# Optimization experiments

Hardware: AMD Instinct MI355X
Metric: run time of the kernel (lower is better)

## Reference

```python
import jax, jax.numpy as jnp
import numpy as np
import math

DM, DP, P = 1024, 128, 256
B, S = 8, 4096

def setup_inputs() -> dict:
    key = jax.random.key(0)
    ks = jax.random.split(key, 7)
    sd = lambda fan_in: 1.0 / math.sqrt(fan_in)
    return {
        "x": jax.random.normal(ks[0], (B, S, DM), jnp.float32),
        "prim_embeds": jax.random.normal(ks[1], (P, DP), jnp.float32),
        "Wq": jax.random.normal(ks[2], (DP, DM), jnp.float32) * sd(DM),
        "Wk": jax.random.normal(ks[3], (DP, DP), jnp.float32) * sd(DP),
        "Wv": jax.random.normal(ks[4], (DP, DP), jnp.float32) * sd(DP),
        "Wo": jax.random.normal(ks[5], (DM, DP), jnp.float32) * sd(DP),
        "gate_w": jax.random.normal(ks[6], (1, DM), jnp.float32) * sd(DM),
        "gate_b": jnp.zeros((1,), jnp.float32),
    }

def reference(x, prim_embeds, Wq, Wk, Wv, Wo, gate_w, gate_b):
    # q: [B,S,dp]; k,v: [P,dp]
    q = jnp.einsum('bsm,pm->bsp', x, Wq)          # p here = d_prim
    k = prim_embeds @ Wk.T                         # [P, dp]
    v = prim_embeds @ Wv.T                         # [P, dp]
    scale = 1.0 / math.sqrt(q.shape[-1])
    scores = jnp.einsum('bsd,pd->bsp', q, k) * scale  # [B,S,P]
    attn = jax.nn.softmax(scores, axis=-1)
    ctx = jnp.einsum('bsp,pd->bsd', attn, v)       # [B,S,dp]
    out = jnp.einsum('bsd,md->bsm', ctx, Wo)       # [B,S,dm]
    gate = jax.nn.sigmoid(jnp.einsum('bsm,om->bso', x, gate_w) + gate_b)  # [B,S,1]
    return gate * out
```

## Files before the change

### kernel.cpp

```cpp
#include <hip/hip_runtime.h>
#include <hip/hip_bf16.h>

typedef unsigned short ushort_t;
typedef __attribute__((ext_vector_type(8))) short short8;
typedef __attribute__((ext_vector_type(8))) unsigned short ushort8;
typedef __attribute__((ext_vector_type(4))) float f32x4;

#define MFMA16(a, b, c) __builtin_amdgcn_mfma_f32_16x16x32_bf16((a), (b), (c), 0, 0, 0)

__device__ __forceinline__ ushort_t f2bf(float f) {
  unsigned int u = __builtin_bit_cast(unsigned int, f);
  u += 0x7FFFu + ((u >> 16) & 1u);
  return (ushort_t)(u >> 16);
}

#define DMdim 1024
#define DPdim 128
#define PPdim 256

#define WQ_ROWS 144
#define WQ_EXT_OFF 0
#define WO_OFF (WQ_ROWS * DMdim)
#define KB_OFF (WO_OFF + DMdim * DPdim)
#define VT_OFF (KB_OFF + PPdim * DPdim)

__global__ void prep_kernel(const float* __restrict__ Wq, const float* __restrict__ Wk,
                            const float* __restrict__ Wv, const float* __restrict__ Wo,
                            const float* __restrict__ gate_w, const float* __restrict__ prim,
                            ushort_t* __restrict__ ws) {
  int idx = blockIdx.x * 256 + threadIdx.x;
  if (idx < WQ_ROWS * DMdim) {
    int r = idx >> 10, m = idx & (DMdim - 1);
    float v = (r < DPdim) ? Wq[r * DMdim + m] : (r == DPdim ? gate_w[m] : 0.f);
    ws[WQ_EXT_OFF + idx] = f2bf(v);
    return;
  }
  idx -= WQ_ROWS * DMdim;
  if (idx < DMdim * DPdim) { ws[WO_OFF + idx] = f2bf(Wo[idx]); return; }
  idx -= DMdim * DPdim;
  if (idx < PPdim * DPdim) {
    int p = idx >> 7, d = idx & (DPdim - 1);
    float s = 0.f;
    for (int j = 0; j < DPdim; ++j) s += prim[p * DPdim + j] * Wk[d * DPdim + j];
    ws[KB_OFF + idx] = f2bf(s);
    return;
  }
  idx -= PPdim * DPdim;
  if (idx < PPdim * DPdim) {
    int p = idx >> 7, d = idx & (DPdim - 1);
    float s = 0.f;
    for (int j = 0; j < DPdim; ++j) s += prim[p * DPdim + j] * Wv[d * DPdim + j];
    ws[VT_OFF + d * PPdim + p] = f2bf(s);
  }
}

#define LDX 72
#define LDQ 136
#define LDA 264
#define LDC 136

__global__ __launch_bounds__(256, 2) void fused_kernel(
    const float* __restrict__ x, const float* __restrict__ gate_b,
    const ushort_t* __restrict__ ws, float* __restrict__ out)
{
  __shared__ __align__(16) ushort_t smem[64 * LDA];
  __shared__ float gate_lds[64];

  const ushort_t* wq_ext = ws + WQ_EXT_OFF;
  const ushort_t* wo_b   = ws + WO_OFF;
  const ushort_t* k_b    = ws + KB_OFF;
  const ushort_t* v_t    = ws + VT_OFF;

  const int tid  = threadIdx.x;
  const int wid  = tid >> 6;
  const int lane = tid & 63;
  const int quad = lane >> 4;
  const int l16  = lane & 15;
  const int tok0 = blockIdx.x * 64;

  f32x4 qacc[9];
  #pragma unroll
  for (int ct = 0; ct < 9; ++ct) qacc[ct] = (f32x4){0.f, 0.f, 0.f, 0.f};

  const int srow = tid >> 2, sseg = tid & 3;

  for (int kc = 0; kc < DMdim; kc += 64) {
    const float4* xv = reinterpret_cast<const float4*>(
        x + (tok0 + srow) * DMdim + kc + sseg * 16);
    float4 f0 = xv[0], f1 = xv[1], f2 = xv[2], f3 = xv[3];
    ushort8 u0, u1;
    u0[0]=f2bf(f0.x); u0[1]=f2bf(f0.y); u0[2]=f2bf(f0.z); u0[3]=f2bf(f0.w);
    u0[4]=f2bf(f1.x); u0[5]=f2bf(f1.y); u0[6]=f2bf(f1.z); u0[7]=f2bf(f1.w);
    u1[0]=f2bf(f2.x); u1[1]=f2bf(f2.y); u1[2]=f2bf(f2.z); u1[3]=f2bf(f2.w);
    u1[4]=f2bf(f3.x); u1[5]=f2bf(f3.y); u1[6]=f2bf(f3.z); u1[7]=f2bf(f3.w);
    *reinterpret_cast<ushort8*>(&smem[srow * LDX + sseg * 16])     = u0;
    *reinterpret_cast<ushort8*>(&smem[srow * LDX + sseg * 16 + 8]) = u1;
    __syncthreads();
    #pragma unroll
    for (int ks = 0; ks < 2; ++ks) {
      short8 a = *reinterpret_cast<const short8*>(
          &smem[(wid * 16 + l16) * LDX + ks * 32 + quad * 8]);
      #pragma unroll
      for (int ct = 0; ct < 9; ++ct) {
        short8 b = *reinterpret_cast<const short8*>(
            &wq_ext[(ct * 16 + l16) * DMdim + kc + ks * 32 + quad * 8]);
        qacc[ct] = MFMA16(a, b, qacc[ct]);
      }
    }
    __syncthreads();
  }

  #pragma unroll
  for (int ct = 0; ct < 8; ++ct)
    #pragma unroll
    for (int r = 0; r < 4; ++r)
      smem[(wid * 16 + quad * 4 + r) * LDQ + ct * 16 + l16] = f2bf(qacc[ct][r]);
  if (l16 == 0) {
    float gb = gate_b[0];
    #pragma unroll
    for (int r = 0; r < 4; ++r) {
      float lg = qacc[8][r] + gb;
      gate_lds[wid * 16 + quad * 4 + r] = 1.f / (1.f + __expf(-lg));
    }
  }
  __syncthreads();

  short8 qa[4];
  #pragma unroll
  for (int k4 = 0; k4 < 4; ++k4)
    qa[k4] = *reinterpret_cast<const short8*>(
        &smem[(wid * 16 + l16) * LDQ + k4 * 32 + quad * 8]);

  f32x4 sacc[16];
  #pragma unroll
  for (int ct = 0; ct < 16; ++ct) sacc[ct] = (f32x4){0.f, 0.f, 0.f, 0.f};
  #pragma unroll
  for (int ct = 0; ct < 16; ++ct)
    #pragma unroll
    for (int k4 = 0; k4 < 4; ++k4) {
      short8 b = *reinterpret_cast<const short8*>(
          &k_b[(ct * 16 + l16) * DPdim + k4 * 32 + quad * 8]);
      sacc[ct] = MFMA16(qa[k4], b, sacc[ct]);
    }

  const float SC = 0.08838834764831845f * 1.44269504088896f;
  float rmax[4], rsum[4], inv[4];
  #pragma unroll
  for (int r = 0; r < 4; ++r) rmax[r] = -3.0e38f;
  #pragma unroll
  for (int ct = 0; ct < 16; ++ct)
    #pragma unroll
    for (int r = 0; r < 4; ++r) rmax[r] = fmaxf(rmax[r], sacc[ct][r]);
  #pragma unroll
  for (int m = 1; m < 16; m <<= 1)
    #pragma unroll
    for (int r = 0; r < 4; ++r) rmax[r] = fmaxf(rmax[r], __shfl_xor(rmax[r], m, 64));
  #pragma unroll
  for (int r = 0; r < 4; ++r) rsum[r] = 0.f;
  #pragma unroll
  for (int ct = 0; ct < 16; ++ct)
    #pragma unroll
    for (int r = 0; r < 4; ++r) {
      float e = exp2f((sacc[ct][r] - rmax[r]) * SC);
      sacc[ct][r] = e;
      rsum[r] += e;
    }
  #pragma unroll
  for (int m = 1; m < 16; m <<= 1)
    #pragma unroll
    for (int r = 0; r < 4; ++r) rsum[r] += __shfl_xor(rsum[r], m, 64);
  #pragma unroll
  for (int r = 0; r < 4; ++r) inv[r] = 1.f / rsum[r];

  __syncthreads();
  #pragma unroll
  for (int ct = 0; ct < 16; ++ct)
    #pragma unroll
    for (int r = 0; r < 4; ++r)
      smem[(wid * 16 + quad * 4 + r) * LDA + ct * 16 + l16] = f2bf(sacc[ct][r]);
  __syncthreads();

  short8 pa[8];
  #pragma unroll
  for (int k8 = 0; k8 < 8; ++k8)
    pa[k8] = *reinterpret_cast<const short8*>(
        &smem[(wid * 16 + l16) * LDA + k8 * 32 + quad * 8]);
  f32x4 cacc[8];
  #pragma unroll
  for (int ct = 0; ct < 8; ++ct) cacc[ct] = (f32x4){0.f, 0.f, 0.f, 0.f};
  #pragma unroll
  for (int ct = 0; ct < 8; ++ct)
    #pragma unroll
    for (int k8 = 0; k8 < 8; ++k8) {
      short8 b = *reinterpret_cast<const short8*>(
          &v_t[(ct * 16 + l16) * PPdim + k8 * 32 + quad * 8]);
      cacc[ct] = MFMA16(pa[k8], b, cacc[ct]);
    }
  __syncthreads();
  #pragma unroll
  for (int ct = 0; ct < 8; ++ct)
    #pragma unroll
    for (int r = 0; r < 4; ++r)
      smem[(wid * 16 + quad * 4 + r) * LDC + ct * 16 + l16] =
          f2bf(cacc[ct][r] * inv[r]);
  __syncthreads();

  short8 ca[4];
  #pragma unroll
  for (int k4 = 0; k4 < 4; ++k4)
    ca[k4] = *reinterpret_cast<const short8*>(
        &smem[(wid * 16 + l16) * LDC + k4 * 32 + quad * 8]);
  float g[4];
  #pragma unroll
  for (int r = 0; r < 4; ++r) g[r] = gate_lds[wid * 16 + quad * 4 + r];

  for (int mc = 0; mc < DMdim; mc += 128) {
    f32x4 oacc[8];
    #pragma unroll
    for (int ct = 0; ct < 8; ++ct) oacc[ct] = (f32x4){0.f, 0.f, 0.f, 0.f};
    #pragma unroll
    for (int ct = 0; ct < 8; ++ct)
      #pragma unroll
      for (int k4 = 0; k4 < 4; ++k4) {
        short8 b = *reinterpret_cast<const short8*>(
            &wo_b[(mc + ct * 16 + l16) * DPdim + k4 * 32 + quad * 8]);
        oacc[ct] = MFMA16(ca[k4], b, oacc[ct]);
      }
    #pragma unroll
    for (int ct = 0; ct < 8; ++ct)
      #pragma unroll
      for (int r = 0; r < 4; ++r)
        out[(tok0 + wid * 16 + quad * 4 + r) * DMdim + mc + ct * 16 + l16] =
            oacc[ct][r] * g[r];
  }
}

extern "C" void kernel_launch(void* const* d_in, const int* in_sizes, int n_in,
                              void* d_out, int out_size, void* d_ws, size_t ws_size,
                              hipStream_t stream) {
  const float* x    = (const float*)d_in[0];
  const float* prim = (const float*)d_in[1];
  const float* Wq   = (const float*)d_in[2];
  const float* Wk   = (const float*)d_in[3];
  const float* Wv   = (const float*)d_in[4];
  const float* Wo   = (const float*)d_in[5];
  const float* gw   = (const float*)d_in[6];
  const float* gb   = (const float*)d_in[7];
  float* out = (float*)d_out;
  ushort_t* ws = (ushort_t*)d_ws;

  prep_kernel<<<344064 / 256, 256, 0, stream>>>(Wq, Wk, Wv, Wo, gw, prim, ws);
  fused_kernel<<<512, 256, 0, stream>>>(x, gb, ws, out);
}
```

Before: 377.8 us.

## Split fused kernel into attention and output-projection kernels with per-wave LDS slabs

Splits the single fused kernel into an attention kernel, which writes bf16 context and gate values to workspace, and a separate output-projection kernel that uses more blocks and higher occupancy. In the attention kernel each wave now loads x directly into MFMA operand registers, which removes the LDS staging and the block-wide barriers. It also gives each wave its own LDS slab. The prep kernel's K/V projections are vectorized with float4. In exchange, the context and gate take an extra round trip through global memory, and per-wave x loads are less coalesced.

```diff
diff --git a/kernel.cpp b/kernel.cpp
--- a/kernel.cpp
+++ b/kernel.cpp
@@ -3,8 +3,8 @@
 
 typedef unsigned short ushort_t;
 typedef __attribute__((ext_vector_type(8))) short short8;
-typedef __attribute__((ext_vector_type(8))) unsigned short ushort8;
 typedef __attribute__((ext_vector_type(4))) float f32x4;
+typedef __attribute__((ext_vector_type(4))) unsigned int uint32x4;
 
 #define MFMA16(a, b, c) __builtin_amdgcn_mfma_f32_16x16x32_bf16((a), (b), (c), 0, 0, 0)
 
@@ -12,6 +12,13 @@
   unsigned int u = __builtin_bit_cast(unsigned int, f);
   u += 0x7FFFu + ((u >> 16) & 1u);
   return (ushort_t)(u >> 16);
+}
+__device__ __forceinline__ unsigned int pack2bf(float a, float b) {
+  unsigned int ua = __builtin_bit_cast(unsigned int, a);
+  unsigned int ub = __builtin_bit_cast(unsigned int, b);
+  ua += 0x7FFFu + ((ua >> 16) & 1u);
+  ub += 0x7FFFu + ((ub >> 16) & 1u);
+  return (ua >> 16) | (ub & 0xFFFF0000u);
 }
 
 #define DMdim 1024
@@ -23,6 +30,8 @@
 #define WO_OFF (WQ_ROWS * DMdim)
 #define KB_OFF (WO_OFF + DMdim * DPdim)
 #define VT_OFF (KB_OFF + PPdim * DPdim)
+#define CTX_OFF (VT_OFF + PPdim * DPdim)
+#define GATE_BYTE_OFF ((size_t)(CTX_OFF + 32768 * DPdim) * 2)
 
 __global__ void prep_kernel(const float* __restrict__ Wq, const float* __restrict__ Wk,
                             const float* __restrict__ Wv, const float* __restrict__ Wo,
@@ -38,36 +47,34 @@
   idx -= WQ_ROWS * DMdim;
   if (idx < DMdim * DPdim) { ws[WO_OFF + idx] = f2bf(Wo[idx]); return; }
   idx -= DMdim * DPdim;
-  if (idx < PPdim * DPdim) {
-    int p = idx >> 7, d = idx & (DPdim - 1);
+  if (idx < 2 * PPdim * DPdim) {
+    bool is_v = idx >= PPdim * DPdim;
+    int e = is_v ? idx - PPdim * DPdim : idx;
+    int p = e >> 7, d = e & (DPdim - 1);
+    const float4* pr = reinterpret_cast<const float4*>(prim + p * DPdim);
+    const float4* wr = reinterpret_cast<const float4*>((is_v ? Wv : Wk) + d * DPdim);
     float s = 0.f;
-    for (int j = 0; j < DPdim; ++j) s += prim[p * DPdim + j] * Wk[d * DPdim + j];
-    ws[KB_OFF + idx] = f2bf(s);
-    return;
-  }
-  idx -= PPdim * DPdim;
-  if (idx < PPdim * DPdim) {
-    int p = idx >> 7, d = idx & (DPdim - 1);
-    float s = 0.f;
-    for (int j = 0; j < DPdim; ++j) s += prim[p * DPdim + j] * Wv[d * DPdim + j];
-    ws[VT_OFF + d * PPdim + p] = f2bf(s);
-  }
-}
-
-#define LDX 72
+    #pragma unroll
+    for (int j = 0; j < DPdim / 4; ++j) {
+      float4 a = pr[j], b = wr[j];
+      s += a.x * b.x + a.y * b.y + a.z * b.z + a.w * b.w;
+    }
+    if (is_v) ws[VT_OFF + d * PPdim + p] = f2bf(s);
+    else      ws[KB_OFF + p * DPdim + d] = f2bf(s);
+  }
+}
+
 #define LDQ 136
 #define LDA 264
-#define LDC 136
-
-__global__ __launch_bounds__(256, 2) void fused_kernel(
+
+__global__ __launch_bounds__(256, 2) void attn_kernel(
     const float* __restrict__ x, const float* __restrict__ gate_b,
-    const ushort_t* __restrict__ ws, float* __restrict__ out)
+    const ushort_t* __restrict__ ws, ushort_t* __restrict__ ctx_out,
+    float* __restrict__ gate_out)
 {
-  __shared__ __align__(16) ushort_t smem[64 * LDA];
-  __shared__ float gate_lds[64];
+  __shared__ __align__(16) ushort_t smem[4 * 16 * LDA];
 
   const ushort_t* wq_ext = ws + WQ_EXT_OFF;
-  const ushort_t* wo_b   = ws + WO_OFF;
   const ushort_t* k_b    = ws + KB_OFF;
   const ushort_t* v_t    = ws + VT_OFF;
 
@@ -76,60 +83,50 @@
   const int lane = tid & 63;
   const int quad = lane >> 4;
   const int l16  = lane & 15;
-  const int tok0 = blockIdx.x * 64;
+  const int tok0 = blockIdx.x * 64 + wid * 16;
+  ushort_t* slab = &smem[wid * 16 * LDA];
 
   f32x4 qacc[9];
   #pragma unroll
   for (int ct = 0; ct < 9; ++ct) qacc[ct] = (f32x4){0.f, 0.f, 0.f, 0.f};
 
-  const int srow = tid >> 2, sseg = tid & 3;
-
-  for (int kc = 0; kc < DMdim; kc += 64) {
-    const float4* xv = reinterpret_cast<const float4*>(
-        x + (tok0 + srow) * DMdim + kc + sseg * 16);
-    float4 f0 = xv[0], f1 = xv[1], f2 = xv[2], f3 = xv[3];
-    ushort8 u0, u1;
-    u0[0]=f2bf(f0.x); u0[1]=f2bf(f0.y); u0[2]=f2bf(f0.z); u0[3]=f2bf(f0.w);
-    u0[4]=f2bf(f1.x); u0[5]=f2bf(f1.y); u0[6]=f2bf(f1.z); u0[7]=f2bf(f1.w);
-    u1[0]=f2bf(f2.x); u1[1]=f2bf(f2.y); u1[2]=f2bf(f2.z); u1[3]=f2bf(f2.w);
-    u1[4]=f2bf(f3.x); u1[5]=f2bf(f3.y); u1[6]=f2bf(f3.z); u1[7]=f2bf(f3.w);
-    *reinterpret_cast<ushort8*>(&smem[srow * LDX + sseg * 16])     = u0;
-    *reinterpret_cast<ushort8*>(&smem[srow * LDX + sseg * 16 + 8]) = u1;
-    __syncthreads();
-    #pragma unroll
-    for (int ks = 0; ks < 2; ++ks) {
-      short8 a = *reinterpret_cast<const short8*>(
-          &smem[(wid * 16 + l16) * LDX + ks * 32 + quad * 8]);
-      #pragma unroll
-      for (int ct = 0; ct < 9; ++ct) {
-        short8 b = *reinterpret_cast<const short8*>(
-            &wq_ext[(ct * 16 + l16) * DMdim + kc + ks * 32 + quad * 8]);
-        qacc[ct] = MFMA16(a, b, qacc[ct]);
-      }
-    }
-    __syncthreads();
-  }
-
-  #pragma unroll
-  for (int ct = 0; ct < 8; ++ct)
-    #pragma unroll
-    for (int r = 0; r < 4; ++r)
-      smem[(wid * 16 + quad * 4 + r) * LDQ + ct * 16 + l16] = f2bf(qacc[ct][r]);
+  const float* xrow = x + (size_t)(tok0 + l16) * DMdim + quad * 8;
+
+  #pragma unroll 4
+  for (int kc = 0; kc < DMdim; kc += 32) {
+    float4 f0 = *reinterpret_cast<const float4*>(xrow + kc);
+    float4 f1 = *reinterpret_cast<const float4*>(xrow + kc + 4);
+    uint32x4 pk;
+    pk[0] = pack2bf(f0.x, f0.y); pk[1] = pack2bf(f0.z, f0.w);
+    pk[2] = pack2bf(f1.x, f1.y); pk[3] = pack2bf(f1.z, f1.w);
+    short8 a = __builtin_bit_cast(short8, pk);
+    #pragma unroll
+    for (int ct = 0; ct < 9; ++ct) {
+      short8 b = *reinterpret_cast<const short8*>(
+          &wq_ext[(size_t)(ct * 16 + l16) * DMdim + kc + quad * 8]);
+      qacc[ct] = MFMA16(a, b, qacc[ct]);
+    }
+  }
+
   if (l16 == 0) {
     float gb = gate_b[0];
     #pragma unroll
     for (int r = 0; r < 4; ++r) {
       float lg = qacc[8][r] + gb;
-      gate_lds[wid * 16 + quad * 4 + r] = 1.f / (1.f + __expf(-lg));
-    }
-  }
-  __syncthreads();
+      gate_out[tok0 + quad * 4 + r] = 1.f / (1.f + __expf(-lg));
+    }
+  }
+
+  #pragma unroll
+  for (int ct = 0; ct < 8; ++ct)
+    #pragma unroll
+    for (int r = 0; r < 4; ++r)
+      slab[(quad * 4 + r) * LDQ + ct * 16 + l16] = f2bf(qacc[ct][r]);
 
   short8 qa[4];
   #pragma unroll
   for (int k4 = 0; k4 < 4; ++k4)
-    qa[k4] = *reinterpret_cast<const short8*>(
-        &smem[(wid * 16 + l16) * LDQ + k4 * 32 + quad * 8]);
+    qa[k4] = *reinterpret_cast<const short8*>(&slab[l16 * LDQ + k4 * 32 + quad * 8]);
 
   f32x4 sacc[16];
   #pragma unroll
@@ -139,7 +136,7 @@
     #pragma unroll
     for (int k4 = 0; k4 < 4; ++k4) {
       short8 b = *reinterpret_cast<const short8*>(
-          &k_b[(ct * 16 + l16) * DPdim + k4 * 32 + quad * 8]);
+          &k_b[(size_t)(ct * 16 + l16) * DPdim + k4 * 32 + quad * 8]);
       sacc[ct] = MFMA16(qa[k4], b, sacc[ct]);
     }
 
@@ -172,19 +169,17 @@
   #pragma unroll
   for (int r = 0; r < 4; ++r) inv[r] = 1.f / rsum[r];
 
-  __syncthreads();
-  #pragma unroll
-  for (int ct = 0; ct < 16; ++ct)
-    #pragma unroll
-    for (int r = 0; r < 4; ++r)
-      smem[(wid * 16 + quad * 4 + r) * LDA + ct * 16 + l16] = f2bf(sacc[ct][r]);
-  __syncthreads();
+  #pragma unroll
+  for (int ct = 0; ct < 16; ++ct)
+    #pragma unroll
+    for (int r = 0; r < 4; ++r)
+      slab[(quad * 4 + r) * LDA + ct * 16 + l16] = f2bf(sacc[ct][r]);
 
   short8 pa[8];
   #pragma unroll
   for (int k8 = 0; k8 < 8; ++k8)
-    pa[k8] = *reinterpret_cast<const short8*>(
-        &smem[(wid * 16 + l16) * LDA + k8 * 32 + quad * 8]);
+    pa[k8] = *reinterpret_cast<const short8*>(&slab[l16 * LDA + k8 * 32 + quad * 8]);
+
   f32x4 cacc[8];
   #pragma unroll
   for (int ct = 0; ct < 8; ++ct) cacc[ct] = (f32x4){0.f, 0.f, 0.f, 0.f};
@@ -193,45 +188,53 @@
     #pragma unroll
     for (int k8 = 0; k8 < 8; ++k8) {
       short8 b = *reinterpret_cast<const short8*>(
-          &v_t[(ct * 16 + l16) * PPdim + k8 * 32 + quad * 8]);
+          &v_t[(size_t)(ct * 16 + l16) * PPdim + k8 * 32 + quad * 8]);
       cacc[ct] = MFMA16(pa[k8], b, cacc[ct]);
     }
-  __syncthreads();
+
   #pragma unroll
   for (int ct = 0; ct < 8; ++ct)
     #pragma unroll
     for (int r = 0; r < 4; ++r)
-      smem[(wid * 16 + quad * 4 + r) * LDC + ct * 16 + l16] =
+      ctx_out[(size_t)(tok0 + quad * 4 + r) * DPdim + ct * 16 + l16] =
           f2bf(cacc[ct][r] * inv[r]);
-  __syncthreads();
+}
+
+__global__ __launch_bounds__(256, 4) void out_kernel(
+    const ushort_t* __restrict__ ctx, const float* __restrict__ gate,
+    const ushort_t* __restrict__ ws, float* __restrict__ out)
+{
+  const ushort_t* wo_b = ws + WO_OFF;
+  const int tid  = threadIdx.x;
+  const int wid  = tid >> 6;
+  const int lane = tid & 63;
+  const int quad = lane >> 4;
+  const int l16  = lane & 15;
+  const int tok0 = blockIdx.x * 32 + (wid & 1) * 16;
+  const int mc0  = (wid >> 1) * 512;
 
   short8 ca[4];
   #pragma unroll
   for (int k4 = 0; k4 < 4; ++k4)
     ca[k4] = *reinterpret_cast<const short8*>(
-        &smem[(wid * 16 + l16) * LDC + k4 * 32 + quad * 8]);
+        &ctx[(size_t)(tok0 + l16) * DPdim + k4 * 32 + quad * 8]);
   float g[4];
   #pragma unroll
-  for (int r = 0; r < 4; ++r) g[r] = gate_lds[wid * 16 + quad * 4 + r];
-
-  for (int mc = 0; mc < DMdim; mc += 128) {
-    f32x4 oacc[8];
-    #pragma unroll
-    for (int ct = 0; ct < 8; ++ct) oacc[ct] = (f32x4){0.f, 0.f, 0.f, 0.f};
-    #pragma unroll
-    for (int ct = 0; ct < 8; ++ct)
-      #pragma unroll
-      for (int k4 = 0; k4 < 4; ++k4) {
-        short8 b = *reinterpret_cast<const short8*>(
-            &wo_b[(mc + ct * 16 + l16) * DPdim + k4 * 32 + quad * 8]);
-        oacc[ct] = MFMA16(ca[k4], b, oacc[ct]);
-      }
-    #pragma unroll
-    for (int ct = 0; ct < 8; ++ct)
-      #pragma unroll
-      for (int r = 0; r < 4; ++r)
-        out[(tok0 + wid * 16 + quad * 4 + r) * DMdim + mc + ct * 16 + l16] =
-            oacc[ct][r] * g[r];
+  for (int r = 0; r < 4; ++r) g[r] = gate[tok0 + quad * 4 + r];
+
+  #pragma unroll 4
+  for (int ct = 0; ct < 32; ++ct) {
+    const int col0 = mc0 + ct * 16;
+    f32x4 oacc = (f32x4){0.f, 0.f, 0.f, 0.f};
+    #pragma unroll
+    for (int k4 = 0; k4 < 4; ++k4) {
+      short8 b = *reinterpret_cast<const short8*>(
+          &wo_b[(size_t)(col0 + l16) * DPdim + k4 * 32 + quad * 8]);
+      oacc = MFMA16(ca[k4], b, oacc);
+    }
+    #pragma unroll
+    for (int r = 0; r < 4; ++r)
+      out[(size_t)(tok0 + quad * 4 + r) * DMdim + col0 + l16] = oacc[r] * g[r];
   }
 }
 
@@ -248,7 +251,10 @@
   const float* gb   = (const float*)d_in[7];
   float* out = (float*)d_out;
   ushort_t* ws = (ushort_t*)d_ws;
+  ushort_t* ctx = ws + CTX_OFF;
+  float* gate = (float*)((char*)d_ws + GATE_BYTE_OFF);
 
   prep_kernel<<<344064 / 256, 256, 0, stream>>>(Wq, Wk, Wv, Wo, gw, prim, ws);
-  fused_kernel<<<512, 256, 0, stream>>>(x, gb, ws, out);
-}
+  attn_kernel<<<512, 256, 0, stream>>>(x, gb, ws, ctx, gate);
+  out_kernel<<<1024, 256, 0, stream>>>(ctx, gate, ws, out);
+}
```

Result: slower. 396.0 us (+4.8%).

## Fold K into Wq and V into Wo to cut per-token GEMM chain

Applied to the files above, without the earlier changes.

Precomputes K·Wq (256x1024 plus the gate row) and Wo·V (1024x256) in prep kernels, so the fused kernel computes scores directly from x and the output directly from the softmax probabilities. This removes the separate Q, context, and two small projection GEMMs per token. Weights are stored pre-swizzled in MFMA fragment order so B loads are contiguous per lane. Warps are split across score columns, with the softmax max and sum reduced across warps through LDS. The trade-off is more MFMA work per token (x@KWq is 1024x272 versus 1024x144) and an extra bf16 rounding on the folded weights.

```diff
diff --git a/kernel.cpp b/kernel.cpp
--- a/kernel.cpp
+++ b/kernel.cpp
@@ -6,232 +6,296 @@
 typedef __attribute__((ext_vector_type(8))) unsigned short ushort8;
 typedef __attribute__((ext_vector_type(4))) float f32x4;
 
-#define MFMA16(a, b, c) __builtin_amdgcn_mfma_f32_16x16x32_bf16((a), (b), (c), 0, 0, 0)
+#define MFMA16(a,b,c) __builtin_amdgcn_mfma_f32_16x16x32_bf16((a),(b),(c),0,0,0)
 
 __device__ __forceinline__ ushort_t f2bf(float f) {
   unsigned int u = __builtin_bit_cast(unsigned int, f);
   u += 0x7FFFu + ((u >> 16) & 1u);
   return (ushort_t)(u >> 16);
 }
-
-#define DMdim 1024
-#define DPdim 128
-#define PPdim 256
-
-#define WQ_ROWS 144
-#define WQ_EXT_OFF 0
-#define WO_OFF (WQ_ROWS * DMdim)
-#define KB_OFF (WO_OFF + DMdim * DPdim)
-#define VT_OFF (KB_OFF + PPdim * DPdim)
-
-__global__ void prep_kernel(const float* __restrict__ Wq, const float* __restrict__ Wk,
-                            const float* __restrict__ Wv, const float* __restrict__ Wo,
-                            const float* __restrict__ gate_w, const float* __restrict__ prim,
-                            ushort_t* __restrict__ ws) {
+__device__ __forceinline__ unsigned int pack2bf(float a, float b) {
+  unsigned int ua = __builtin_bit_cast(unsigned int, a);
+  unsigned int ub = __builtin_bit_cast(unsigned int, b);
+  ua += 0x7FFFu + ((ua >> 16) & 1u);
+  ub += 0x7FFFu + ((ub >> 16) & 1u);
+  return (ua >> 16) | (ub & 0xFFFF0000u);
+}
+
+#define DMd 1024
+#define DPd 128
+#define PPd 256
+
+#define KWQ_OFF 0
+#define KWQ_SIZE (8*17*4*512)
+#define VWO_OFF KWQ_SIZE
+#define VWO_SIZE (64*8*512)
+#define KV_BYTE_OFF ((size_t)(KWQ_SIZE + VWO_SIZE) * 2)
+
+__global__ void prep1_kernel(const float* __restrict__ prim, const float* __restrict__ Wk,
+                             const float* __restrict__ Wv, ushort_t* __restrict__ ws) {
+  float* kf = (float*)((char*)ws + KV_BYTE_OFF);
+  float* vf = kf + 32768;
   int idx = blockIdx.x * 256 + threadIdx.x;
-  if (idx < WQ_ROWS * DMdim) {
-    int r = idx >> 10, m = idx & (DMdim - 1);
-    float v = (r < DPdim) ? Wq[r * DMdim + m] : (r == DPdim ? gate_w[m] : 0.f);
-    ws[WQ_EXT_OFF + idx] = f2bf(v);
-    return;
-  }
-  idx -= WQ_ROWS * DMdim;
-  if (idx < DMdim * DPdim) { ws[WO_OFF + idx] = f2bf(Wo[idx]); return; }
-  idx -= DMdim * DPdim;
-  if (idx < PPdim * DPdim) {
-    int p = idx >> 7, d = idx & (DPdim - 1);
-    float s = 0.f;
-    for (int j = 0; j < DPdim; ++j) s += prim[p * DPdim + j] * Wk[d * DPdim + j];
-    ws[KB_OFF + idx] = f2bf(s);
-    return;
-  }
-  idx -= PPdim * DPdim;
-  if (idx < PPdim * DPdim) {
-    int p = idx >> 7, d = idx & (DPdim - 1);
-    float s = 0.f;
-    for (int j = 0; j < DPdim; ++j) s += prim[p * DPdim + j] * Wv[d * DPdim + j];
-    ws[VT_OFF + d * PPdim + p] = f2bf(s);
-  }
-}
-
-#define LDX 72
-#define LDQ 136
-#define LDA 264
-#define LDC 136
+  int mat = idx >> 15, rem = idx & 32767;
+  int p = rem >> 7, d = rem & 127;
+  const float4* pr = (const float4*)(prim + p * 128);
+  const float4* wr = (const float4*)((mat ? Wv : Wk) + d * 128);
+  float s0 = 0.f, s1 = 0.f;
+  #pragma unroll
+  for (int j = 0; j < 32; j += 2) {
+    float4 a = pr[j], b = wr[j];
+    s0 += a.x*b.x + a.y*b.y + a.z*b.z + a.w*b.w;
+    float4 a2 = pr[j+1], b2 = wr[j+1];
+    s1 += a2.x*b2.x + a2.y*b2.y + a2.z*b2.z + a2.w*b2.w;
+  }
+  (mat ? vf : kf)[rem] = s0 + s1;
+}
+
+__global__ void prep2_kernel(const float* __restrict__ Wq, const float* __restrict__ Wo,
+                             const float* __restrict__ gate_w, ushort_t* __restrict__ ws) {
+  const float* kf = (const float*)((const char*)ws + KV_BYTE_OFF);
+  const float* vf = kf + 32768;
+  const int b = blockIdx.x, t = threadIdx.x;
+  if (b < 68) {
+    const int p  = (b >> 2) * 16 + (t >> 4);
+    const int m0 = (b & 3) * 256 + (t & 15) * 16;
+    float acc[16];
+    #pragma unroll
+    for (int j = 0; j < 16; ++j) acc[j] = 0.f;
+    if (p < 256) {
+      const float* kp = kf + p * 128;
+      for (int d = 0; d < 128; ++d) {
+        float kv = kp[d];
+        const float4* wr = (const float4*)(Wq + (size_t)d * 1024 + m0);
+        #pragma unroll
+        for (int q = 0; q < 4; ++q) {
+          float4 w = wr[q];
+          acc[q*4+0] += kv * w.x; acc[q*4+1] += kv * w.y;
+          acc[q*4+2] += kv * w.z; acc[q*4+3] += kv * w.w;
+        }
+      }
+    } else if (p == 256) {
+      #pragma unroll
+      for (int j = 0; j < 16; ++j) acc[j] = gate_w[m0 + j];
+    }
+    const int ct = p >> 4, l16p = p & 15;
+    const int c = m0 >> 7, k4 = (m0 >> 5) & 3, q0 = (m0 >> 3) & 3;
+    ushort8 u0, u1;
+    #pragma unroll
+    for (int j = 0; j < 8; ++j) { u0[j] = f2bf(acc[j]); u1[j] = f2bf(acc[8+j]); }
+    size_t base = ((size_t)(c * 17 + ct) * 4 + k4) * 512;
+    *(ushort8*)&ws[KWQ_OFF + base + (size_t)(q0 * 16 + l16p) * 8]       = u0;
+    *(ushort8*)&ws[KWQ_OFF + base + (size_t)((q0 + 1) * 16 + l16p) * 8] = u1;
+  } else {
+    __shared__ float vs[16 * 128];
+    const int bb = b - 68;
+    const int p0 = (bb >> 2) * 16;
+    const int m  = (bb & 3) * 256 + t;
+    {
+      int row = t >> 4, col = (t & 15) * 8;
+      const float4* src = (const float4*)(vf + (p0 + row) * 128 + col);
+      float4 a0 = src[0], a1 = src[1];
+      *(float4*)&vs[row * 128 + col]     = a0;
+      *(float4*)&vs[row * 128 + col + 4] = a1;
+    }
+    __syncthreads();
+    float acc[16];
+    #pragma unroll
+    for (int j = 0; j < 16; ++j) acc[j] = 0.f;
+    const float4* wr = (const float4*)(Wo + (size_t)m * 128);
+    for (int d4 = 0; d4 < 32; ++d4) {
+      float4 w = wr[d4];
+      #pragma unroll
+      for (int pp = 0; pp < 16; ++pp) {
+        float4 v4 = *(const float4*)&vs[pp * 128 + d4 * 4];
+        acc[pp] += w.x*v4.x + w.y*v4.y + w.z*v4.z + w.w*v4.w;
+      }
+    }
+    const int ctg = m >> 4, l16m = m & 15;
+    ushort8 u0, u1;
+    #pragma unroll
+    for (int j = 0; j < 8; ++j) { u0[j] = f2bf(acc[j]); u1[j] = f2bf(acc[8+j]); }
+    const int pA = p0, pB = p0 + 8;
+    *(ushort8*)&ws[VWO_OFF + ((size_t)(ctg*8 + (pA>>5))*512) + (size_t)(((pA>>3)&3)*16 + l16m)*8] = u0;
+    *(ushort8*)&ws[VWO_OFF + ((size_t)(ctg*8 + (pB>>5))*512) + (size_t)(((pB>>3)&3)*16 + l16m)*8] = u1;
+  }
+}
+
+#define LDX 136
+#define LDSLAB 264
 
 __global__ __launch_bounds__(256, 2) void fused_kernel(
     const float* __restrict__ x, const float* __restrict__ gate_b,
     const ushort_t* __restrict__ ws, float* __restrict__ out)
 {
-  __shared__ __align__(16) ushort_t smem[64 * LDA];
-  __shared__ float gate_lds[64];
-
-  const ushort_t* wq_ext = ws + WQ_EXT_OFF;
-  const ushort_t* wo_b   = ws + WO_OFF;
-  const ushort_t* k_b    = ws + KB_OFF;
-  const ushort_t* v_t    = ws + VT_OFF;
-
-  const int tid  = threadIdx.x;
-  const int wid  = tid >> 6;
-  const int lane = tid & 63;
-  const int quad = lane >> 4;
-  const int l16  = lane & 15;
+  __shared__ __align__(16) char smem[64 * LDSLAB * 2 + 64 * 4 * 4 * 2 + 64 * 4];
+  ushort_t* xt       = (ushort_t*)smem;
+  ushort_t* slab     = (ushort_t*)smem;
+  float*    pmax     = (float*)(smem + 64 * LDSLAB * 2);
+  float*    psum     = pmax + 256;
+  float*    gate_lds = psum + 256;
+
+  const int t = threadIdx.x, wid = t >> 6, lane = t & 63;
+  const int quad = lane >> 4, l16 = lane & 15;
   const int tok0 = blockIdx.x * 64;
 
-  f32x4 qacc[9];
-  #pragma unroll
-  for (int ct = 0; ct < 9; ++ct) qacc[ct] = (f32x4){0.f, 0.f, 0.f, 0.f};
-
-  const int srow = tid >> 2, sseg = tid & 3;
-
-  for (int kc = 0; kc < DMdim; kc += 64) {
-    const float4* xv = reinterpret_cast<const float4*>(
-        x + (tok0 + srow) * DMdim + kc + sseg * 16);
-    float4 f0 = xv[0], f1 = xv[1], f2 = xv[2], f3 = xv[3];
-    ushort8 u0, u1;
-    u0[0]=f2bf(f0.x); u0[1]=f2bf(f0.y); u0[2]=f2bf(f0.z); u0[3]=f2bf(f0.w);
-    u0[4]=f2bf(f1.x); u0[5]=f2bf(f1.y); u0[6]=f2bf(f1.z); u0[7]=f2bf(f1.w);
-    u1[0]=f2bf(f2.x); u1[1]=f2bf(f2.y); u1[2]=f2bf(f2.z); u1[3]=f2bf(f2.w);
-    u1[4]=f2bf(f3.x); u1[5]=f2bf(f3.y); u1[6]=f2bf(f3.z); u1[7]=f2bf(f3.w);
-    *reinterpret_cast<ushort8*>(&smem[srow * LDX + sseg * 16])     = u0;
-    *reinterpret_cast<ushort8*>(&smem[srow * LDX + sseg * 16 + 8]) = u1;
+  f32x4 acc[4][5];
+  #pragma unroll
+  for (int rt = 0; rt < 4; ++rt)
+    #pragma unroll
+    for (int ctl = 0; ctl < 5; ++ctl) acc[rt][ctl] = (f32x4){0.f,0.f,0.f,0.f};
+
+  for (int c = 0; c < 8; ++c) {
+    if (c) __syncthreads();
+    #pragma unroll
+    for (int i = 0; i < 8; ++i) {
+      int flat = i * 1024 + t * 4;
+      int row = flat >> 7, col = flat & 127;
+      float4 f = *(const float4*)(x + (size_t)(tok0 + row) * 1024 + c * 128 + col);
+      unsigned int pk0 = pack2bf(f.x, f.y), pk1 = pack2bf(f.z, f.w);
+      unsigned long long dv = (unsigned long long)pk0 | ((unsigned long long)pk1 << 32);
+      *(unsigned long long*)&xt[row * LDX + col] = dv;
+    }
     __syncthreads();
     #pragma unroll
-    for (int ks = 0; ks < 2; ++ks) {
-      short8 a = *reinterpret_cast<const short8*>(
-          &smem[(wid * 16 + l16) * LDX + ks * 32 + quad * 8]);
-      #pragma unroll
-      for (int ct = 0; ct < 9; ++ct) {
-        short8 b = *reinterpret_cast<const short8*>(
-            &wq_ext[(ct * 16 + l16) * DMdim + kc + ks * 32 + quad * 8]);
-        qacc[ct] = MFMA16(a, b, qacc[ct]);
+    for (int k4 = 0; k4 < 4; ++k4) {
+      short8 a[4];
+      #pragma unroll
+      for (int rt = 0; rt < 4; ++rt)
+        a[rt] = *(const short8*)&xt[(rt * 16 + l16) * LDX + k4 * 32 + quad * 8];
+      #pragma unroll
+      for (int ctl = 0; ctl < 5; ++ctl) {
+        if (ctl == 4 && wid != 3) continue;
+        const int ct = wid * 4 + ctl;
+        short8 bfr = *(const short8*)&ws[KWQ_OFF +
+            ((size_t)(c * 17 + ct) * 4 + k4) * 512 + (size_t)lane * 8];
+        #pragma unroll
+        for (int rt = 0; rt < 4; ++rt) acc[rt][ctl] = MFMA16(a[rt], bfr, acc[rt][ctl]);
       }
     }
-    __syncthreads();
-  }
-
-  #pragma unroll
-  for (int ct = 0; ct < 8; ++ct)
-    #pragma unroll
-    for (int r = 0; r < 4; ++r)
-      smem[(wid * 16 + quad * 4 + r) * LDQ + ct * 16 + l16] = f2bf(qacc[ct][r]);
+  }
+
+  const float SC = 0.08838834764831845f * 1.44269504088896f;
+  float Mx[4][4];
+  #pragma unroll
+  for (int rt = 0; rt < 4; ++rt)
+    #pragma unroll
+    for (int r = 0; r < 4; ++r) {
+      float m = acc[rt][0][r];
+      #pragma unroll
+      for (int ctl = 1; ctl < 4; ++ctl) m = fmaxf(m, acc[rt][ctl][r]);
+      #pragma unroll
+      for (int msk = 1; msk < 16; msk <<= 1) m = fmaxf(m, __shfl_xor(m, msk, 64));
+      Mx[rt][r] = m;
+    }
   if (l16 == 0) {
-    float gb = gate_b[0];
+    #pragma unroll
+    for (int rt = 0; rt < 4; ++rt)
+      #pragma unroll
+      for (int r = 0; r < 4; ++r)
+        pmax[(rt * 16 + quad * 4 + r) * 4 + wid] = Mx[rt][r];
+  }
+  __syncthreads();
+  float Mf[4][4];
+  #pragma unroll
+  for (int rt = 0; rt < 4; ++rt)
     #pragma unroll
     for (int r = 0; r < 4; ++r) {
-      float lg = qacc[8][r] + gb;
-      gate_lds[wid * 16 + quad * 4 + r] = 1.f / (1.f + __expf(-lg));
+      f32x4 pm = *(f32x4*)&pmax[(rt * 16 + quad * 4 + r) * 4];
+      Mf[rt][r] = fmaxf(fmaxf(pm[0], pm[1]), fmaxf(pm[2], pm[3]));
+    }
+  float Sm[4][4];
+  #pragma unroll
+  for (int rt = 0; rt < 4; ++rt)
+    #pragma unroll
+    for (int r = 0; r < 4; ++r) Sm[rt][r] = 0.f;
+  #pragma unroll
+  for (int rt = 0; rt < 4; ++rt)
+    #pragma unroll
+    for (int ctl = 0; ctl < 4; ++ctl)
+      #pragma unroll
+      for (int r = 0; r < 4; ++r) {
+        float e = exp2f((acc[rt][ctl][r] - Mf[rt][r]) * SC);
+        acc[rt][ctl][r] = e;
+        Sm[rt][r] += e;
+      }
+  #pragma unroll
+  for (int rt = 0; rt < 4; ++rt)
+    #pragma unroll
+    for (int r = 0; r < 4; ++r) {
+      #pragma unroll
+      for (int msk = 1; msk < 16; msk <<= 1) Sm[rt][r] += __shfl_xor(Sm[rt][r], msk, 64);
+    }
+  if (l16 == 0) {
+    #pragma unroll
+    for (int rt = 0; rt < 4; ++rt)
+      #pragma unroll
+      for (int r = 0; r < 4; ++r)
+        psum[(rt * 16 + quad * 4 + r) * 4 + wid] = Sm[rt][r];
+    if (wid == 3) {
+      float gb = gate_b[0];
+      #pragma unroll
+      for (int rt = 0; rt < 4; ++rt)
+        #pragma unroll
+        for (int r = 0; r < 4; ++r) {
+          float lg = acc[rt][4][r] + gb;
+          gate_lds[rt * 16 + quad * 4 + r] = 1.f / (1.f + __expf(-lg));
+        }
     }
   }
   __syncthreads();
-
-  short8 qa[4];
-  #pragma unroll
-  for (int k4 = 0; k4 < 4; ++k4)
-    qa[k4] = *reinterpret_cast<const short8*>(
-        &smem[(wid * 16 + l16) * LDQ + k4 * 32 + quad * 8]);
-
-  f32x4 sacc[16];
-  #pragma unroll
-  for (int ct = 0; ct < 16; ++ct) sacc[ct] = (f32x4){0.f, 0.f, 0.f, 0.f};
-  #pragma unroll
-  for (int ct = 0; ct < 16; ++ct)
-    #pragma unroll
-    for (int k4 = 0; k4 < 4; ++k4) {
-      short8 b = *reinterpret_cast<const short8*>(
-          &k_b[(ct * 16 + l16) * DPdim + k4 * 32 + quad * 8]);
-      sacc[ct] = MFMA16(qa[k4], b, sacc[ct]);
-    }
-
-  const float SC = 0.08838834764831845f * 1.44269504088896f;
-  float rmax[4], rsum[4], inv[4];
-  #pragma unroll
-  for (int r = 0; r < 4; ++r) rmax[r] = -3.0e38f;
-  #pragma unroll
-  for (int ct = 0; ct < 16; ++ct)
-    #pragma unroll
-    for (int r = 0; r < 4; ++r) rmax[r] = fmaxf(rmax[r], sacc[ct][r]);
-  #pragma unroll
-  for (int m = 1; m < 16; m <<= 1)
-    #pragma unroll
-    for (int r = 0; r < 4; ++r) rmax[r] = fmaxf(rmax[r], __shfl_xor(rmax[r], m, 64));
-  #pragma unroll
-  for (int r = 0; r < 4; ++r) rsum[r] = 0.f;
-  #pragma unroll
-  for (int ct = 0; ct < 16; ++ct)
+  float inv[4][4];
+  #pragma unroll
+  for (int rt = 0; rt < 4; ++rt)
     #pragma unroll
     for (int r = 0; r < 4; ++r) {
-      float e = exp2f((sacc[ct][r] - rmax[r]) * SC);
-      sacc[ct][r] = e;
-      rsum[r] += e;
-    }
-  #pragma unroll
-  for (int m = 1; m < 16; m <<= 1)
-    #pragma unroll
-    for (int r = 0; r < 4; ++r) rsum[r] += __shfl_xor(rsum[r], m, 64);
-  #pragma unroll
-  for (int r = 0; r < 4; ++r) inv[r] = 1.f / rsum[r];
-
+      f32x4 ps = *(f32x4*)&psum[(rt * 16 + quad * 4 + r) * 4];
+      inv[rt][r] = 1.f / (ps[0] + ps[1] + ps[2] + ps[3]);
+    }
+
+  #pragma unroll
+  for (int rt = 0; rt < 4; ++rt)
+    #pragma unroll
+    for (int ctl = 0; ctl < 4; ++ctl)
+      #pragma unroll
+      for (int r = 0; r < 4; ++r)
+        slab[(rt * 16 + quad * 4 + r) * LDSLAB + (wid * 4 + ctl) * 16 + l16] =
+            f2bf(acc[rt][ctl][r] * inv[rt][r]);
   __syncthreads();
-  #pragma unroll
-  for (int ct = 0; ct < 16; ++ct)
-    #pragma unroll
-    for (int r = 0; r < 4; ++r)
-      smem[(wid * 16 + quad * 4 + r) * LDA + ct * 16 + l16] = f2bf(sacc[ct][r]);
-  __syncthreads();
-
-  short8 pa[8];
-  #pragma unroll
-  for (int k8 = 0; k8 < 8; ++k8)
-    pa[k8] = *reinterpret_cast<const short8*>(
-        &smem[(wid * 16 + l16) * LDA + k8 * 32 + quad * 8]);
-  f32x4 cacc[8];
-  #pragma unroll
-  for (int ct = 0; ct < 8; ++ct) cacc[ct] = (f32x4){0.f, 0.f, 0.f, 0.f};
-  #pragma unroll
-  for (int ct = 0; ct < 8; ++ct)
-    #pragma unroll
-    for (int k8 = 0; k8 < 8; ++k8) {
-      short8 b = *reinterpret_cast<const short8*>(
-          &v_t[(ct * 16 + l16) * PPdim + k8 * 32 + quad * 8]);
-      cacc[ct] = MFMA16(pa[k8], b, cacc[ct]);
-    }
-  __syncthreads();
-  #pragma unroll
-  for (int ct = 0; ct < 8; ++ct)
-    #pragma unroll
-    for (int r = 0; r < 4; ++r)
-      smem[(wid * 16 + quad * 4 + r) * LDC + ct * 16 + l16] =
-          f2bf(cacc[ct][r] * inv[r]);
-  __syncthreads();
-
-  short8 ca[4];
-  #pragma unroll
-  for (int k4 = 0; k4 < 4; ++k4)
-    ca[k4] = *reinterpret_cast<const short8*>(
-        &smem[(wid * 16 + l16) * LDC + k4 * 32 + quad * 8]);
-  float g[4];
-  #pragma unroll
-  for (int r = 0; r < 4; ++r) g[r] = gate_lds[wid * 16 + quad * 4 + r];
-
-  for (int mc = 0; mc < DMdim; mc += 128) {
-    f32x4 oacc[8];
-    #pragma unroll
-    for (int ct = 0; ct < 8; ++ct) oacc[ct] = (f32x4){0.f, 0.f, 0.f, 0.f};
-    #pragma unroll
-    for (int ct = 0; ct < 8; ++ct)
-      #pragma unroll
-      for (int k4 = 0; k4 < 4; ++k4) {
-        short8 b = *reinterpret_cast<const short8*>(
-            &wo_b[(mc + ct * 16 + l16) * DPdim + k4 * 32 + quad * 8]);
-        oacc[ct] = MFMA16(ca[k4], b, oacc[ct]);
-      }
-    #pragma unroll
-    for (int ct = 0; ct < 8; ++ct)
+
+  short8 af[4][8];
+  #pragma unroll
+  for (int rt = 0; rt < 4; ++rt)
+    #pragma unroll
+    for (int k8 = 0; k8 < 8; ++k8)
+      af[rt][k8] = *(const short8*)&slab[(rt * 16 + l16) * LDSLAB + k8 * 32 + quad * 8];
+  float g[4][4];
+  #pragma unroll
+  for (int rt = 0; rt < 4; ++rt)
+    #pragma unroll
+    for (int r = 0; r < 4; ++r) g[rt][r] = gate_lds[rt * 16 + quad * 4 + r];
+
+  const int n0 = wid * 256;
+  for (int nt = 0; nt < 16; ++nt) {
+    const int ctg = (n0 >> 4) + nt;
+    short8 bf[8];
+    #pragma unroll
+    for (int k8 = 0; k8 < 8; ++k8)
+      bf[k8] = *(const short8*)&ws[VWO_OFF + ((size_t)(ctg * 8 + k8) * 512) + (size_t)lane * 8];
+    f32x4 oa[4];
+    #pragma unroll
+    for (int rt = 0; rt < 4; ++rt) oa[rt] = (f32x4){0.f,0.f,0.f,0.f};
+    #pragma unroll
+    for (int rt = 0; rt < 4; ++rt)
+      #pragma unroll
+      for (int k8 = 0; k8 < 8; ++k8)
+        oa[rt] = MFMA16(af[rt][k8], bf[k8], oa[rt]);
+    #pragma unroll
+    for (int rt = 0; rt < 4; ++rt)
       #pragma unroll
       for (int r = 0; r < 4; ++r)
-        out[(tok0 + wid * 16 + quad * 4 + r) * DMdim + mc + ct * 16 + l16] =
-            oacc[ct][r] * g[r];
+        out[(size_t)(tok0 + rt * 16 + quad * 4 + r) * 1024 + n0 + nt * 16 + l16] =
+            oa[rt][r] * g[rt][r];
   }
 }
 
@@ -249,6 +313,7 @@
   float* out = (float*)d_out;
   ushort_t* ws = (ushort_t*)d_ws;
 
-  prep_kernel<<<344064 / 256, 256, 0, stream>>>(Wq, Wk, Wv, Wo, gw, prim, ws);
+  prep1_kernel<<<256, 256, 0, stream>>>(prim, Wk, Wv, ws);
+  prep2_kernel<<<132, 256, 0, stream>>>(Wq, Wo, gw, ws);
   fused_kernel<<<512, 256, 0, stream>>>(x, gb, ws, out);
 }
```

Measured after the change: 352.4 us. 1.07x faster.
